# Performance work log

Hardware: AMD Instinct MI355X
Metric: run time of the kernel (lower is better)

Reference implementation:

```python
import jax, jax.numpy as jnp
import numpy as np

D_MODEL = 1024
N_HEAD = 16
DEPTH = D_MODEL // N_HEAD
B, N = 2, 2048


def setup_inputs() -> dict:
    key = jax.random.key(0)
    ks = jax.random.split(key, 9)
    s = 1.0 / np.sqrt(D_MODEL)
    inp = {
        "input": jax.random.normal(ks[0], (B, N, D_MODEL), dtype=jnp.float32),
        # causal boolean mask; True = keep (module masks where mask is False)
        "mask": jnp.broadcast_to(jnp.tril(jnp.ones((N, N), dtype=bool)), (B, N, N)),
        "Wq": jax.random.uniform(ks[1], (D_MODEL, D_MODEL), jnp.float32, -s, s),
        "bq": jax.random.uniform(ks[2], (D_MODEL,), jnp.float32, -s, s),
        "Wk": jax.random.uniform(ks[3], (D_MODEL, D_MODEL), jnp.float32, -s, s),
        "bk": jax.random.uniform(ks[4], (D_MODEL,), jnp.float32, -s, s),
        "Wv": jax.random.uniform(ks[5], (D_MODEL, D_MODEL), jnp.float32, -s, s),
        "bv": jax.random.uniform(ks[6], (D_MODEL,), jnp.float32, -s, s),
        "Wo": jax.random.uniform(ks[7], (D_MODEL, D_MODEL), jnp.float32, -s, s),
        "bo": jax.random.uniform(ks[8], (D_MODEL,), jnp.float32, -s, s),
    }
    return inp


def reference(input, mask, Wq, bq, Wk, bk, Wv, bv, Wo, bo):
    b, n, _ = input.shape
    # projections (dropout in eval mode = identity)
    q = (input @ Wq.T + bq).reshape(b, n, N_HEAD, DEPTH)
    k = (input @ Wk.T + bk).reshape(b, n, N_HEAD, DEPTH)
    v = (input @ Wv.T + bv).reshape(b, n, N_HEAD, DEPTH)
    scale = 1.0 / np.sqrt(DEPTH)
    # scores: [b, h, q, k]
    scores = jnp.einsum("bqhd,bkhd->bhqk", q, k) * scale
    scores = jnp.where(mask[:, None, :, :], scores, -jnp.inf)
    attn = jax.nn.softmax(scores, axis=-1)
    out = jnp.einsum("bhqk,bkhd->bqhd", attn, v).reshape(b, n, D_MODEL)
    return out @ Wo.T + bo
```

## Files before the change

kernel.cpp:

```cpp
#include <hip/hip_runtime.h>
#include <stdint.h>

#define DM 1024
#define NH 16
#define DEPTH 64
#define BB 2
#define NN 2048
#define ROWS (BB*NN)

typedef __attribute__((ext_vector_type(8))) short short8;
typedef __attribute__((ext_vector_type(4))) short short4v;
typedef __attribute__((ext_vector_type(4))) float f32x4;

static __device__ __forceinline__ unsigned short f2b(float f) {
  unsigned u = __float_as_uint(f);
  u += 0x7fffu + ((u >> 16) & 1u);
  return (unsigned short)(u >> 16);
}

__global__ void cvt5_kernel(const float* __restrict__ s0, const float* __restrict__ s1,
                            const float* __restrict__ s2, const float* __restrict__ s3,
                            const float* __restrict__ s4,
                            unsigned short* __restrict__ d0, unsigned short* __restrict__ d1,
                            unsigned short* __restrict__ d2, unsigned short* __restrict__ d3,
                            unsigned short* __restrict__ d4) {
  const float* src; unsigned short* dst; int n4;
  const int seg = blockIdx.y;
  if (seg == 0)      { src = s0; dst = d0; n4 = ROWS * DM / 4; }
  else if (seg == 1) { src = s1; dst = d1; n4 = DM * DM / 4; }
  else if (seg == 2) { src = s2; dst = d2; n4 = DM * DM / 4; }
  else if (seg == 3) { src = s3; dst = d3; n4 = DM * DM / 4; }
  else               { src = s4; dst = d4; n4 = DM * DM / 4; }
  int i = blockIdx.x * blockDim.x + threadIdx.x;
  int stride = gridDim.x * blockDim.x;
  for (; i < n4; i += stride) {
    float4 v = reinterpret_cast<const float4*>(src)[i];
    short4v o;
    o.x = (short)f2b(v.x); o.y = (short)f2b(v.y);
    o.z = (short)f2b(v.z); o.w = (short)f2b(v.w);
    reinterpret_cast<short4v*>(dst)[i] = o;
  }
}

template<int OUTF32>
__global__ __launch_bounds__(256)
void gemm_bt(const unsigned short* __restrict__ A, const unsigned short* __restrict__ B,
             const float* __restrict__ bias0, const float* __restrict__ bias1,
             const float* __restrict__ bias2, float sc0,
             float* __restrict__ Cf, unsigned short* __restrict__ Cb,
             int K, int N) {
  __shared__ unsigned short As[128 * 32];
  __shared__ unsigned short Bs[128 * 32];
  const int tid = threadIdx.x;
  const int lane = tid & 63;
  const int w = tid >> 6;
  const int wr = w >> 1, wc = w & 1;
  const int l15 = lane & 15, l4 = lane >> 4;
  const int m0 = blockIdx.y * 128, n0 = blockIdx.x * 128;
  f32x4 acc[4][4] = {};
  const int nkt = K >> 5;
  for (int kt = 0; kt < nkt; ++kt) {
    const int kbase = kt * 32;
#pragma unroll
    for (int i = 0; i < 2; ++i) {
      int c = tid + i * 256;
      int row = c >> 2, ko = (c & 3) * 8;
      __builtin_amdgcn_global_load_lds(
          (__attribute__((address_space(1))) void*)(A + (size_t)(m0 + row) * K + kbase + ko),
          (__attribute__((address_space(3))) void*)((char*)As + c * 16), 16, 0, 0);
      __builtin_amdgcn_global_load_lds(
          (__attribute__((address_space(1))) void*)(B + (size_t)(n0 + row) * K + kbase + ko),
          (__attribute__((address_space(3))) void*)((char*)Bs + c * 16), 16, 0, 0);
    }
    __syncthreads();
    short8 a[4], b[4];
#pragma unroll
    for (int mi = 0; mi < 4; ++mi)
      a[mi] = *reinterpret_cast<const short8*>(&As[(wr * 64 + mi * 16 + l15) * 32 + l4 * 8]);
#pragma unroll
    for (int ni = 0; ni < 4; ++ni)
      b[ni] = *reinterpret_cast<const short8*>(&Bs[(wc * 64 + ni * 16 + l15) * 32 + l4 * 8]);
#pragma unroll
    for (int mi = 0; mi < 4; ++mi)
#pragma unroll
      for (int ni = 0; ni < 4; ++ni)
        acc[mi][ni] = __builtin_amdgcn_mfma_f32_16x16x32_bf16(a[mi], b[ni], acc[mi][ni], 0, 0, 0);
    __syncthreads();
  }
  const float* bp = bias0; int boff = 0;
  if (n0 >= 2048)      { bp = bias2; boff = 2048; }
  else if (n0 >= 1024) { bp = bias1; boff = 1024; }
  const float sc = (n0 < 1024) ? sc0 : 1.0f;
#pragma unroll
  for (int ni = 0; ni < 4; ++ni) {
    int col = n0 + wc * 64 + ni * 16 + l15;
    float bv = bp[col - boff];
#pragma unroll
    for (int mi = 0; mi < 4; ++mi) {
      f32x4 v = acc[mi][ni];
#pragma unroll
      for (int r = 0; r < 4; ++r) {
        int row = m0 + wr * 64 + mi * 16 + l4 * 4 + r;
        float outv = (v[r] + bv) * sc;
        if (OUTF32) Cf[(size_t)row * N + col] = outv;
        else        Cb[(size_t)row * N + col] = f2b(outv);
      }
    }
  }
}

__global__ __launch_bounds__(256)
void vtrans_kernel(const unsigned short* __restrict__ qkv, unsigned short* __restrict__ vt) {
  const int bh = blockIdx.y, b = bh >> 4, h = bh & 15;
  const int n0 = blockIdx.x * 64;
  __shared__ unsigned short t[64][72];
  const unsigned short* src = qkv + (size_t)(b * NN) * 3072 + 2048 + h * 64;
#pragma unroll
  for (int i = 0; i < 2; ++i) {
    int c = threadIdx.x + i * 256;
    int row = c >> 3, d0 = (c & 7) * 8;
    short8 v = *reinterpret_cast<const short8*>(src + (size_t)(n0 + row) * 3072 + d0);
#pragma unroll
    for (int j = 0; j < 8; ++j) t[d0 + j][row] = (unsigned short)v[j];
  }
  __syncthreads();
  unsigned short* dst = vt + ((size_t)(b * NH + h) * DEPTH) * NN + n0;
#pragma unroll
  for (int i = 0; i < 2; ++i) {
    int c = threadIdx.x + i * 256;
    int d = c >> 3, nn0 = (c & 7) * 8;
    short8 v;
#pragma unroll
    for (int j = 0; j < 8; ++j) v[j] = (short)t[d][nn0 + j];
    *reinterpret_cast<short8*>(dst + (size_t)d * NN + nn0) = v;
  }
}

__global__ __launch_bounds__(256, 4)
void attn_kernel(const unsigned short* __restrict__ qkv, const unsigned short* __restrict__ vt,
                 unsigned short* __restrict__ aout) {
  const int tid = threadIdx.x, lane = tid & 63, w = tid >> 6;
  const int l15 = lane & 15, l4 = lane >> 4;
  const int blk = blockIdx.x;
  const int g = (blk & 7) * 128 + (blk >> 3);
  const int bh = g >> 5;
  const int jj = g & 31;
  const int pi = 2 * jj + (w >> 1);
  const int half = w & 1;
  const int batch = bh >> 4, h = bh & 15;
  const unsigned short* Qp  = qkv + (size_t)(batch * NN) * 3072 + h * 64;
  const unsigned short* Kp  = Qp + 1024;
  const unsigned short* Vtp = vt + (size_t)(batch * NH + h) * DEPTH * NN;
  __shared__ unsigned short plds[4][16 * 40];
  __shared__ float mergeO[4][16][68];
  __shared__ float mergeM[4][16];
  __shared__ float mergeL[4][16];
  unsigned short* pw = plds[w];

  for (int ip = 0; ip < 2; ++ip) {
    const int qt = ip ? (127 - pi) : pi;
    const int qp0 = qt * 16;
    const int nkt = (qt >> 1) + 1;
    const int kmid = (nkt + 1) >> 1;
    const int kb = half ? kmid : 0;
    const int ke = half ? nkt : kmid;
    short8 qf[2];
#pragma unroll
    for (int kk = 0; kk < 2; ++kk)
      qf[kk] = *reinterpret_cast<const short8*>(
          Qp + (size_t)(qp0 + l15) * 3072 + kk * 32 + l4 * 8);
    f32x4 o[4] = {};
    float m = -3.0e38f, l = 0.0f;
    short8 kf[2][2];
    if (kb < ke) {
#pragma unroll
      for (int cf = 0; cf < 2; ++cf)
#pragma unroll
        for (int kk = 0; kk < 2; ++kk)
          kf[cf][kk] = *reinterpret_cast<const short8*>(
              Kp + (size_t)(kb * 32 + cf * 16 + l15) * 3072 + kk * 32 + l4 * 8);
    }

    for (int kt = kb; kt < ke; ++kt) {
      const int k0 = kt * 32;
      f32x4 s[2];
#pragma unroll
      for (int cf = 0; cf < 2; ++cf) {
        f32x4 z = {};
        z = __builtin_amdgcn_mfma_f32_16x16x32_bf16(kf[cf][0], qf[0], z, 0, 0, 0);
        s[cf] = __builtin_amdgcn_mfma_f32_16x16x32_bf16(kf[cf][1], qf[1], z, 0, 0, 0);
      }
      short8 vf[4];
#pragma unroll
      for (int dn = 0; dn < 4; ++dn)
        vf[dn] = *reinterpret_cast<const short8*>(
            Vtp + (size_t)(dn * 16 + l15) * NN + k0 + l4 * 8);
      const int kn = (kt + 1 < ke) ? k0 + 32 : k0;
#pragma unroll
      for (int cf = 0; cf < 2; ++cf)
#pragma unroll
        for (int kk = 0; kk < 2; ++kk)
          kf[cf][kk] = *reinterpret_cast<const short8*>(
              Kp + (size_t)(kn + cf * 16 + l15) * 3072 + kk * 32 + l4 * 8);
      float p[2][4];
      const bool diag = (kt == nkt - 1);
#pragma unroll
      for (int cf = 0; cf < 2; ++cf)
#pragma unroll
        for (int r = 0; r < 4; ++r) {
          float x = s[cf][r];
          if (diag && (k0 + cf * 16 + l4 * 4 + r > qp0 + l15)) x = -3.0e38f;
          p[cf][r] = x;
        }
      float pm = fmaxf(
          fmaxf(fmaxf(p[0][0], p[0][1]), fmaxf(p[0][2], p[0][3])),
          fmaxf(fmaxf(p[1][0], p[1][1]), fmaxf(p[1][2], p[1][3])));
      pm = fmaxf(pm, __shfl_xor(pm, 16));
      pm = fmaxf(pm, __shfl_xor(pm, 32));
      if (!__all(pm <= m + 11.5f)) {
        const float mn = fmaxf(m, pm);
        const float al = exp2f(m - mn);
        m = mn;
        l *= al;
#pragma unroll
        for (int dn = 0; dn < 4; ++dn)
#pragma unroll
          for (int r = 0; r < 4; ++r) o[dn][r] *= al;
      }
      float ps = 0.0f;
#pragma unroll
      for (int cf = 0; cf < 2; ++cf)
#pragma unroll
        for (int r = 0; r < 4; ++r) {
          p[cf][r] = exp2f(p[cf][r] - m);
          ps += p[cf][r];
        }
      ps += __shfl_xor(ps, 16);
      ps += __shfl_xor(ps, 32);
      l += ps;
#pragma unroll
      for (int cf = 0; cf < 2; ++cf)
#pragma unroll
        for (int hh = 0; hh < 2; ++hh) {
          unsigned pk = (unsigned)f2b(p[cf][2 * hh]) |
                        ((unsigned)f2b(p[cf][2 * hh + 1]) << 16);
          *reinterpret_cast<unsigned*>(&pw[l15 * 40 + cf * 16 + l4 * 4 + 2 * hh]) = pk;
        }
      short8 pf = *reinterpret_cast<const short8*>(&pw[l15 * 40 + l4 * 8]);
#pragma unroll
      for (int dn = 0; dn < 4; ++dn)
        o[dn] = __builtin_amdgcn_mfma_f32_16x16x32_bf16(vf[dn], pf, o[dn], 0, 0, 0);
    }
    if (l4 == 0) { mergeM[w][l15] = m; mergeL[w][l15] = l; }
#pragma unroll
    for (int dn = 0; dn < 4; ++dn)
      *reinterpret_cast<f32x4*>(&mergeO[w][l15][dn * 16 + l4 * 4]) = o[dn];
    __syncthreads();
    if (half == 0) {
      const float m1 = mergeM[w ^ 1][l15];
      const float l1 = mergeL[w ^ 1][l15];
      const float mn = fmaxf(m, m1);
      const float a0 = exp2f(m - mn);
      const float a1 = exp2f(m1 - mn);
      const float inv = 1.0f / (l * a0 + l1 * a1);
      const int row = batch * NN + qp0 + l15;
#pragma unroll
      for (int dn = 0; dn < 4; ++dn) {
        f32x4 o1 = *reinterpret_cast<const f32x4*>(&mergeO[w ^ 1][l15][dn * 16 + l4 * 4]);
        short4v ov;
#pragma unroll
        for (int r = 0; r < 4; ++r)
          ov[r] = (short)f2b((o[dn][r] * a0 + o1[r] * a1) * inv);
        *reinterpret_cast<short4v*>(&aout[(size_t)row * DM + h * 64 + dn * 16 + l4 * 4]) = ov;
      }
    }
    __syncthreads();
  }
}

extern "C" void kernel_launch(void* const* d_in, const int* in_sizes, int n_in,
                              void* d_out, int out_size, void* d_ws, size_t ws_size,
                              hipStream_t stream) {
  const float* X  = (const float*)d_in[0];
  const float* Wq = (const float*)d_in[2];
  const float* bq = (const float*)d_in[3];
  const float* Wk = (const float*)d_in[4];
  const float* bk = (const float*)d_in[5];
  const float* Wv = (const float*)d_in[6];
  const float* bv = (const float*)d_in[7];
  const float* Wo = (const float*)d_in[8];
  const float* bo = (const float*)d_in[9];
  float* out = (float*)d_out;

  char* ws = (char*)d_ws;
  unsigned short* Xb     = (unsigned short*)(ws);
  unsigned short* Wstack = (unsigned short*)(ws + 8ull  * 1024 * 1024);
  unsigned short* Wob    = (unsigned short*)(ws + 14ull * 1024 * 1024);
  unsigned short* QKV    = (unsigned short*)(ws + 16ull * 1024 * 1024);
  unsigned short* Vt     = (unsigned short*)(ws + 40ull * 1024 * 1024);
  unsigned short* AOut   = (unsigned short*)(ws + 48ull * 1024 * 1024);

  cvt5_kernel<<<dim3(128, 5), 256, 0, stream>>>(X, Wq, Wk, Wv, Wo,
                                                Xb, Wstack, Wstack + 1024 * 1024,
                                                Wstack + 2 * 1024 * 1024, Wob);

  gemm_bt<0><<<dim3(24, 32), 256, 0, stream>>>(Xb, Wstack, bq, bk, bv, 0.18033688f,
                                               nullptr, QKV, DM, 3072);
  vtrans_kernel<<<dim3(32, 32), 256, 0, stream>>>(QKV, Vt);
  attn_kernel<<<dim3(1024), 256, 0, stream>>>(QKV, Vt, AOut);
  gemm_bt<1><<<dim3(8, 32), 256, 0, stream>>>(AOut, Wob, bo, bo, bo, 1.0f,
                                              out, nullptr, DM, DM);
}
```

Before: 310.7 us.

## Pre-pack K and V into MFMA fragment order for contiguous attention loads

Replaces the V-transpose kernel with a fragpack kernel that writes both K and V tiles in per-lane MFMA fragment order, 32-key blocks of 2048 elements each. The attention kernel then loads K and V fragments with fully contiguous 16-byte loads instead of strided rows across the 3072-wide QKV buffer. This is meant to improve memory coalescing and cache-line use in the attention inner loop. The cost is an extra packing pass over K and a reshuffled workspace that reuses the Xb and Wstack regions after they are consumed.

Measured after the change: 257.4 us. 1.21x faster.

```diff
diff --git a/kernel.cpp b/kernel.cpp
--- a/kernel.cpp
+++ b/kernel.cpp
@@ -110,34 +110,52 @@
 }
 
 __global__ __launch_bounds__(256)
-void vtrans_kernel(const unsigned short* __restrict__ qkv, unsigned short* __restrict__ vt) {
-  const int bh = blockIdx.y, b = bh >> 4, h = bh & 15;
-  const int n0 = blockIdx.x * 64;
-  __shared__ unsigned short t[64][72];
-  const unsigned short* src = qkv + (size_t)(b * NN) * 3072 + 2048 + h * 64;
-#pragma unroll
-  for (int i = 0; i < 2; ++i) {
-    int c = threadIdx.x + i * 256;
-    int row = c >> 3, d0 = (c & 7) * 8;
-    short8 v = *reinterpret_cast<const short8*>(src + (size_t)(n0 + row) * 3072 + d0);
-#pragma unroll
-    for (int j = 0; j < 8; ++j) t[d0 + j][row] = (unsigned short)v[j];
+void fragpack_kernel(const unsigned short* __restrict__ qkv,
+                     unsigned short* __restrict__ kfrag,
+                     unsigned short* __restrict__ vfrag) {
+  const int tid = threadIdx.x, lane = tid & 63, w = tid >> 6;
+  const int l15 = lane & 15, l4 = lane >> 4;
+  const int u = blockIdx.x * 4 + w;
+  const int bh = u >> 6, kt = u & 63;
+  const int batch = bh >> 4, h = bh & 15;
+  const int k0 = kt * 32;
+  const int lo = (l15 * 4 + l4) * 8;
+  __shared__ unsigned short tv[4][32][72];
+
+  const unsigned short* Kg = qkv + (size_t)(batch * NN + k0) * 3072 + 1024 + h * 64;
+  unsigned short* Kd = kfrag + (size_t)u * 2048;
+#pragma unroll
+  for (int cf = 0; cf < 2; ++cf)
+#pragma unroll
+    for (int kk = 0; kk < 2; ++kk) {
+      short8 v = *reinterpret_cast<const short8*>(
+          Kg + (size_t)(cf * 16 + l15) * 3072 + kk * 32 + l4 * 8);
+      *reinterpret_cast<short8*>(Kd + (cf * 2 + kk) * 512 + lo) = v;
+    }
+
+  const unsigned short* Vg = qkv + (size_t)(batch * NN + k0) * 3072 + 2048 + h * 64;
+#pragma unroll
+  for (int i = 0; i < 4; ++i) {
+    int q = i * 64 + lane;
+    int row = q >> 3, doff = (q & 7) * 8;
+    short8 v = *reinterpret_cast<const short8*>(Vg + (size_t)row * 3072 + doff);
+    *reinterpret_cast<short8*>(&tv[w][row][doff]) = v;
   }
   __syncthreads();
-  unsigned short* dst = vt + ((size_t)(b * NH + h) * DEPTH) * NN + n0;
-#pragma unroll
-  for (int i = 0; i < 2; ++i) {
-    int c = threadIdx.x + i * 256;
-    int d = c >> 3, nn0 = (c & 7) * 8;
+  unsigned short* Vd = vfrag + (size_t)u * 2048;
+#pragma unroll
+  for (int dn = 0; dn < 4; ++dn) {
     short8 v;
 #pragma unroll
-    for (int j = 0; j < 8; ++j) v[j] = (short)t[d][nn0 + j];
-    *reinterpret_cast<short8*>(dst + (size_t)d * NN + nn0) = v;
+    for (int j = 0; j < 8; ++j) v[j] = (short)tv[w][l4 * 8 + j][dn * 16 + l15];
+    *reinterpret_cast<short8*>(Vd + dn * 512 + lo) = v;
   }
 }
 
 __global__ __launch_bounds__(256, 4)
-void attn_kernel(const unsigned short* __restrict__ qkv, const unsigned short* __restrict__ vt,
+void attn_kernel(const unsigned short* __restrict__ qkv,
+                 const unsigned short* __restrict__ kfrag,
+                 const unsigned short* __restrict__ vfrag,
                  unsigned short* __restrict__ aout) {
   const int tid = threadIdx.x, lane = tid & 63, w = tid >> 6;
   const int l15 = lane & 15, l4 = lane >> 4;
@@ -149,8 +167,9 @@
   const int half = w & 1;
   const int batch = bh >> 4, h = bh & 15;
   const unsigned short* Qp  = qkv + (size_t)(batch * NN) * 3072 + h * 64;
-  const unsigned short* Kp  = Qp + 1024;
-  const unsigned short* Vtp = vt + (size_t)(batch * NH + h) * DEPTH * NN;
+  const unsigned short* Kfb = kfrag + (size_t)(bh * 64) * 2048;
+  const unsigned short* Vfb = vfrag + (size_t)(bh * 64) * 2048;
+  const int lo = (l15 * 4 + l4) * 8;
   __shared__ unsigned short plds[4][16 * 40];
   __shared__ float mergeO[4][16][68];
   __shared__ float mergeM[4][16];
@@ -178,7 +197,7 @@
 #pragma unroll
         for (int kk = 0; kk < 2; ++kk)
           kf[cf][kk] = *reinterpret_cast<const short8*>(
-              Kp + (size_t)(kb * 32 + cf * 16 + l15) * 3072 + kk * 32 + l4 * 8);
+              Kfb + (size_t)kb * 2048 + (cf * 2 + kk) * 512 + lo);
     }
 
     for (int kt = kb; kt < ke; ++kt) {
@@ -194,14 +213,14 @@
 #pragma unroll
       for (int dn = 0; dn < 4; ++dn)
         vf[dn] = *reinterpret_cast<const short8*>(
-            Vtp + (size_t)(dn * 16 + l15) * NN + k0 + l4 * 8);
-      const int kn = (kt + 1 < ke) ? k0 + 32 : k0;
+            Vfb + (size_t)kt * 2048 + dn * 512 + lo);
+      const int knt = (kt + 1 < ke) ? kt + 1 : kt;
 #pragma unroll
       for (int cf = 0; cf < 2; ++cf)
 #pragma unroll
         for (int kk = 0; kk < 2; ++kk)
           kf[cf][kk] = *reinterpret_cast<const short8*>(
-              Kp + (size_t)(kn + cf * 16 + l15) * 3072 + kk * 32 + l4 * 8);
+              Kfb + (size_t)knt * 2048 + (cf * 2 + kk) * 512 + lo);
       float p[2][4];
       const bool diag = (kt == nkt - 1);
 #pragma unroll
@@ -294,11 +313,12 @@
 
   char* ws = (char*)d_ws;
   unsigned short* Xb     = (unsigned short*)(ws);
+  unsigned short* Kfrag  = (unsigned short*)(ws);
   unsigned short* Wstack = (unsigned short*)(ws + 8ull  * 1024 * 1024);
-  unsigned short* Wob    = (unsigned short*)(ws + 14ull * 1024 * 1024);
-  unsigned short* QKV    = (unsigned short*)(ws + 16ull * 1024 * 1024);
-  unsigned short* Vt     = (unsigned short*)(ws + 40ull * 1024 * 1024);
-  unsigned short* AOut   = (unsigned short*)(ws + 48ull * 1024 * 1024);
+  unsigned short* Vfrag  = (unsigned short*)(ws + 8ull  * 1024 * 1024);
+  unsigned short* Wob    = (unsigned short*)(ws + 16ull * 1024 * 1024);
+  unsigned short* QKV    = (unsigned short*)(ws + 18ull * 1024 * 1024);
+  unsigned short* AOut   = (unsigned short*)(ws + 42ull * 1024 * 1024);
 
   cvt5_kernel<<<dim3(128, 5), 256, 0, stream>>>(X, Wq, Wk, Wv, Wo,
                                                 Xb, Wstack, Wstack + 1024 * 1024,
@@ -306,8 +326,8 @@
 
   gemm_bt<0><<<dim3(24, 32), 256, 0, stream>>>(Xb, Wstack, bq, bk, bv, 0.18033688f,
                                                nullptr, QKV, DM, 3072);
-  vtrans_kernel<<<dim3(32, 32), 256, 0, stream>>>(QKV, Vt);
-  attn_kernel<<<dim3(1024), 256, 0, stream>>>(QKV, Vt, AOut);
+  fragpack_kernel<<<dim3(512), 256, 0, stream>>>(QKV, Kfrag, Vfrag);
+  attn_kernel<<<dim3(1024), 256, 0, stream>>>(QKV, Kfrag, Vfrag, AOut);
   gemm_bt<1><<<dim3(8, 32), 256, 0, stream>>>(AOut, Wob, bo, bo, bo, 1.0f,
                                               out, nullptr, DM, DM);
 }
```
